# Kernel optimization log

Measured on AMD Instinct MI355X. Metric: run time of the kernel, lower is better.

The kernel has to match this reference:

```python
import jax, jax.numpy as jnp
import numpy as np

B, N, C = 4, 2048, 1024
H = 16
D = C // H
FF = 4096
EPS = 1e-6


def _layernorm(x, g, b):
    mu = jnp.mean(x, axis=-1, keepdims=True)
    var = jnp.mean(jnp.square(x - mu), axis=-1, keepdims=True)
    return (x - mu) * jax.lax.rsqrt(var + EPS) * g + b


def setup_inputs() -> dict:
    key = jax.random.key(0)
    ks = jax.random.split(key, 8)
    s = 0.02
    x = jax.random.normal(ks[0], (B, N, C), dtype=jnp.float32)
    mask = jnp.tril(jnp.ones((N, N), dtype=bool))[None, None]  # causal [1,1,N,N]
    return {
        "x": x,
        "mask": mask,
        "qkv_w": jax.random.normal(ks[1], (3 * C, C), jnp.float32) * s,
        "qkv_b": jnp.zeros((3 * C,), jnp.float32),
        "proj_w": jax.random.normal(ks[2], (C, C), jnp.float32) * s,
        "proj_b": jnp.zeros((C,), jnp.float32),
        "ln1_g": jnp.ones((C,), jnp.float32),
        "ln1_b": jnp.zeros((C,), jnp.float32),
        "ln2_g": jnp.ones((C,), jnp.float32),
        "ln2_b": jnp.zeros((C,), jnp.float32),
        "w1": jax.random.normal(ks[3], (FF, C), jnp.float32) * s,
        "w2": jax.random.normal(ks[4], (C, FF), jnp.float32) * s,
        "w3": jax.random.normal(ks[5], (FF, C), jnp.float32) * s,
    }


def reference(x, mask, qkv_w, qkv_b, proj_w, proj_b, ln1_g, ln1_b, ln2_g, ln2_b, w1, w2, w3):
    # --- attention sub-block (pre-norm) ---
    h = _layernorm(x, ln1_g, ln1_b)
    qkv = h @ qkv_w.T + qkv_b                      # [B,N,3C]
    qkv = qkv.reshape(B, N, 3, H, D).transpose(2, 0, 3, 1, 4)  # [3,B,H,N,D]
    q, k, v = qkv[0], qkv[1], qkv[2]
    scale = D ** -0.5
    attn = jnp.einsum("bhnd,bhmd->bhnm", q, k) * scale
    attn = jnp.where(mask, attn, -jnp.inf)
    attn = jax.nn.softmax(attn, axis=-1)
    o = jnp.einsum("bhnm,bhmd->bhnd", attn, v)
    o = o.transpose(0, 2, 1, 3).reshape(B, N, C)
    o = o @ proj_w.T + proj_b
    x = x + o  # dropout is identity in eval mode
    # --- SwiGLU MLP sub-block (pre-norm) ---
    h = _layernorm(x, ln2_g, ln2_b)
    m = (jax.nn.silu(h @ w1.T) * (h @ w3.T)) @ w2.T
    return x + m
```

## Files before the change

### kernel.cpp

```cpp
#include <hip/hip_runtime.h>
#include <hip/hip_bf16.h>
#include <stdint.h>

#define NB   4
#define NSEQ 2048
#define NC   1024
#define NH   16
#define ND   64
#define NFF  4096
#define NM   (NB*NSEQ)

typedef __attribute__((ext_vector_type(8))) short short8v;
typedef __attribute__((ext_vector_type(4))) short short4v;
typedef __attribute__((ext_vector_type(4))) float f32x4;

#define GPTR(p) ((const __attribute__((address_space(1))) void*)(p))
#define LPTR(p) ((__attribute__((address_space(3))) void*)(p))

__device__ __forceinline__ short f2bf(float f){
  unsigned u = __builtin_bit_cast(unsigned, f);
  u += 0x7fffu + ((u >> 16) & 1u);
  return (short)(u >> 16);
}
__device__ __forceinline__ float bf2f(short h){
  unsigned u = ((unsigned)(unsigned short)h) << 16;
  return __builtin_bit_cast(float, u);
}
__device__ __forceinline__ f32x4 mfma16x32(short8v a, short8v b, f32x4 c){
  return __builtin_amdgcn_mfma_f32_16x16x32_bf16(a, b, c, 0, 0, 0);
}
__device__ __forceinline__ f32x4 mfma16x16(short4v a, short4v b, f32x4 c){
  return __builtin_amdgcn_mfma_f32_16x16x16bf16_1k(a, b, c, 0, 0, 0);
}
__device__ __forceinline__ short4v pack4bf(f32x4 v){
  __hip_bfloat162 a = __float22bfloat162_rn(float2{v[0], v[1]});
  __hip_bfloat162 b = __float22bfloat162_rn(float2{v[2], v[3]});
  short4v r;
  __builtin_memcpy(&r, &a, 4);
  __builtin_memcpy(((char*)&r) + 4, &b, 4);
  return r;
}

__global__ __launch_bounds__(256) void prep_kernel(
    const float* __restrict__ qkv_w, const float* __restrict__ proj_w,
    const float* __restrict__ w1, const float* __restrict__ w3,
    const float* __restrict__ w2,
    short* __restrict__ wqkv, short* __restrict__ wproj,
    short* __restrict__ w1b, short* __restrict__ w3b, short* __restrict__ w2b,
    const float* __restrict__ x, const float* __restrict__ g,
    const float* __restrict__ bta, short* __restrict__ out){
  int blk = blockIdx.x;
  int tid = threadIdx.x;
  if (blk < 16384){
    const float* src; short* dst; int off;
    if      (blk <  3072){ src = qkv_w;  dst = wqkv;  off = blk; }
    else if (blk <  4096){ src = proj_w; dst = wproj; off = blk - 3072; }
    else if (blk <  8192){ src = w1;     dst = w1b;   off = blk - 4096; }
    else if (blk < 12288){ src = w3;     dst = w3b;   off = blk - 8192; }
    else                 { src = w2;     dst = w2b;   off = blk - 12288; }
    int i = (off * 256 + tid) * 4;
    float4 v = *(const float4*)(src + i);
    short4v r = { f2bf(v.x), f2bf(v.y), f2bf(v.z), f2bf(v.w) };
    *(short4v*)(dst + i) = r;
    return;
  }
  int row = blk - 16384;
  int lane = tid & 63, w = tid >> 6;
  const float4* xr = (const float4*)(x + (size_t)row * NC);
  float4 v = xr[tid];
  float s1 = v.x + v.y + v.z + v.w;
  float s2 = v.x*v.x + v.y*v.y + v.z*v.z + v.w*v.w;
  #pragma unroll
  for (int off = 32; off; off >>= 1){
    s1 += __shfl_xor(s1, off);
    s2 += __shfl_xor(s2, off);
  }
  __shared__ float red[8];
  if (lane == 0){ red[w] = s1; red[4 + w] = s2; }
  __syncthreads();
  s1 = red[0] + red[1] + red[2] + red[3];
  s2 = red[4] + red[5] + red[6] + red[7];
  float mean = s1 * (1.0f / NC);
  float var  = s2 * (1.0f / NC) - mean * mean;
  float inv  = rsqrtf(var + 1e-6f);
  float4 gv = ((const float4*)g)[tid];
  float4 bv = ((const float4*)bta)[tid];
  short4v o = { f2bf((v.x - mean) * inv * gv.x + bv.x),
                f2bf((v.y - mean) * inv * gv.y + bv.y),
                f2bf((v.z - mean) * inv * gv.z + bv.z),
                f2bf((v.w - mean) * inv * gv.w + bv.w) };
  *(short4v*)(out + (size_t)row * NC + tid * 4) = o;
}

__global__ __launch_bounds__(256) void ln_kernel(const float* __restrict__ x,
                                                 const float* __restrict__ g,
                                                 const float* __restrict__ bta,
                                                 short* __restrict__ out){
  int row = blockIdx.x;
  int tid = threadIdx.x;
  int lane = tid & 63, w = tid >> 6;
  const float4* xr = (const float4*)(x + (size_t)row * NC);
  float4 v = xr[tid];
  float s1 = v.x + v.y + v.z + v.w;
  float s2 = v.x*v.x + v.y*v.y + v.z*v.z + v.w*v.w;
  #pragma unroll
  for (int off = 32; off; off >>= 1){
    s1 += __shfl_xor(s1, off);
    s2 += __shfl_xor(s2, off);
  }
  __shared__ float red[8];
  if (lane == 0){ red[w] = s1; red[4 + w] = s2; }
  __syncthreads();
  s1 = red[0] + red[1] + red[2] + red[3];
  s2 = red[4] + red[5] + red[6] + red[7];
  float mean = s1 * (1.0f / NC);
  float var  = s2 * (1.0f / NC) - mean * mean;
  float inv  = rsqrtf(var + 1e-6f);
  float4 gv = ((const float4*)g)[tid];
  float4 bv = ((const float4*)bta)[tid];
  short4v o = { f2bf((v.x - mean) * inv * gv.x + bv.x),
                f2bf((v.y - mean) * inv * gv.y + bv.y),
                f2bf((v.z - mean) * inv * gv.z + bv.z),
                f2bf((v.w - mean) * inv * gv.w + bv.w) };
  *(short4v*)(out + (size_t)row * NC + tid * 4) = o;
}

template<bool HAS_BIAS, bool HAS_RES, bool OUT_BF16, bool QKV_V>
__global__ __launch_bounds__(256, 3) void gemm_bt(const short* __restrict__ A,
                                                  const short* __restrict__ Bm,
                                                  const float* __restrict__ bias,
                                                  const float* __restrict__ res,
                                                  void* __restrict__ outp,
                                                  short* __restrict__ vt,
                                                  int Nc, int K){
  __shared__ short Al[128 * 64];
  __shared__ short Bl[128 * 64];
  int tid = threadIdx.x;
  int gx = gridDim.x, nwg = gx * gridDim.y;
  int wg = blockIdx.y * gx + blockIdx.x;
  int swz = (wg & 7) * (nwg >> 3) + (wg >> 3);
  int m0 = (swz / gx) * 128, n0 = (swz % gx) * 128;
  const short* Ag = A + (size_t)m0 * K;
  const short* Bg = Bm + (size_t)n0 * K;
  int lane = tid & 63, wid = tid >> 6;
  int wm = (wid >> 1) * 64, wn = (wid & 1) * 64;
  int qd = lane >> 4, l15 = lane & 15;

  f32x4 acc[4][4] = {};

  for (int k0 = 0; k0 < K; k0 += 64){
    __syncthreads();
    #pragma unroll
    for (int i = 0; i < 4; i++){
      int cg = (wid * 4 + i) * 64 + lane;
      int r  = cg >> 3, c = cg & 7;
      int sc = (c ^ (r & 7)) << 3;
      __builtin_amdgcn_global_load_lds(GPTR(Ag + (size_t)r * K + k0 + sc),
                                       LPTR(&Al[cg * 8]), 16, 0, 0);
      __builtin_amdgcn_global_load_lds(GPTR(Bg + (size_t)r * K + k0 + sc),
                                       LPTR(&Bl[cg * 8]), 16, 0, 0);
    }
    __syncthreads();
    #pragma unroll
    for (int kk = 0; kk < 2; kk++){
      short8v a[4], b[4];
      #pragma unroll
      for (int t = 0; t < 4; t++){
        int r = wm + t * 16 + l15;
        a[t] = *(const short8v*)&Al[r * 64 + (((kk * 4 + qd) ^ (r & 7)) << 3)];
      }
      #pragma unroll
      for (int t = 0; t < 4; t++){
        int r = wn + t * 16 + l15;
        b[t] = *(const short8v*)&Bl[r * 64 + (((kk * 4 + qd) ^ (r & 7)) << 3)];
      }
      #pragma unroll
      for (int i = 0; i < 4; i++)
        #pragma unroll
        for (int j = 0; j < 4; j++)
          acc[i][j] = mfma16x32(a[i], b[j], acc[i][j]);
    }
  }

  #pragma unroll
  for (int ti = 0; ti < 4; ti++){
    #pragma unroll
    for (int tj = 0; tj < 4; tj++){
      int col = n0 + wn + tj * 16 + l15;
      float bv = HAS_BIAS ? bias[col] : 0.0f;
      if (QKV_V && col >= 2048){
        int row0 = m0 + wm + ti * 16 + qd * 4;
        int hh = (col - 2048) >> 6, dd = col & 63;
        int bb = row0 >> 11, nn = row0 & 2047;
        f32x4 v = { acc[ti][tj][0] + bv, acc[ti][tj][1] + bv,
                    acc[ti][tj][2] + bv, acc[ti][tj][3] + bv };
        *(short4v*)(vt + (((size_t)(bb * 16 + hh) * 64 + dd) << 11) + nn) = pack4bf(v);
      } else {
        #pragma unroll
        for (int r = 0; r < 4; r++){
          int row = m0 + wm + ti * 16 + qd * 4 + r;
          float v = acc[ti][tj][r] + bv;
          size_t idx = (size_t)row * Nc + col;
          if (HAS_RES) v += res[idx];
          if (OUT_BF16) ((short*)outp)[idx] = f2bf(v);
          else          ((float*)outp)[idx] = v;
        }
      }
    }
  }
}

__global__ __launch_bounds__(256, 2) void gemm_ff13(const short* __restrict__ A,
                                                    const short* __restrict__ B1m,
                                                    const short* __restrict__ B3m,
                                                    short* __restrict__ outp){
  __shared__ short Al [128 * 64];
  __shared__ short B1l[128 * 64];
  __shared__ short B3l[128 * 64];
  int tid = threadIdx.x;
  int gx = gridDim.x;
  int wg = blockIdx.y * gx + blockIdx.x;
  int xcd = wg & 7, idx = wg >> 3;
  int npx = gx >> 3;
  int n0 = (xcd * npx + idx % npx) * 128;
  int m0 = (idx / npx) * 128;
  const short* Ag  = A   + (size_t)m0 * NC;
  const short* B1g = B1m + (size_t)n0 * NC;
  const short* B3g = B3m + (size_t)n0 * NC;
  int lane = tid & 63, wid = tid >> 6;
  int wm = (wid >> 1) * 64, wn = (wid & 1) * 64;
  int qd = lane >> 4, l15 = lane & 15;

  f32x4 acc1[4][4] = {}, acc3[4][4] = {};

  for (int k0 = 0; k0 < NC; k0 += 64){
    __syncthreads();
    #pragma unroll
    for (int i = 0; i < 4; i++){
      int cg = (wid * 4 + i) * 64 + lane;
      int r  = cg >> 3, c = cg & 7;
      int sc = (c ^ (r & 7)) << 3;
      __builtin_amdgcn_global_load_lds(GPTR(Ag + (size_t)r * NC + k0 + sc),
                                       LPTR(&Al[cg * 8]), 16, 0, 0);
      __builtin_amdgcn_global_load_lds(GPTR(B1g + (size_t)r * NC + k0 + sc),
                                       LPTR(&B1l[cg * 8]), 16, 0, 0);
      __builtin_amdgcn_global_load_lds(GPTR(B3g + (size_t)r * NC + k0 + sc),
                                       LPTR(&B3l[cg * 8]), 16, 0, 0);
    }
    __syncthreads();
    #pragma unroll
    for (int kk = 0; kk < 2; kk++){
      short8v a[4], b1[4], b3[4];
      #pragma unroll
      for (int t = 0; t < 4; t++){
        int r = wm + t * 16 + l15;
        a[t] = *(const short8v*)&Al[r * 64 + (((kk * 4 + qd) ^ (r & 7)) << 3)];
      }
      #pragma unroll
      for (int t = 0; t < 4; t++){
        int r = wn + t * 16 + l15;
        int co = ((kk * 4 + qd) ^ (r & 7)) << 3;
        b1[t] = *(const short8v*)&B1l[r * 64 + co];
        b3[t] = *(const short8v*)&B3l[r * 64 + co];
      }
      #pragma unroll
      for (int i = 0; i < 4; i++)
        #pragma unroll
        for (int j = 0; j < 4; j++){
          acc1[i][j] = mfma16x32(a[i], b1[j], acc1[i][j]);
          acc3[i][j] = mfma16x32(a[i], b3[j], acc3[i][j]);
        }
    }
  }

  #pragma unroll
  for (int ti = 0; ti < 4; ti++){
    #pragma unroll
    for (int tj = 0; tj < 4; tj++){
      int col = n0 + wn + tj * 16 + l15;
      #pragma unroll
      for (int r = 0; r < 4; r++){
        int row = m0 + wm + ti * 16 + qd * 4 + r;
        float v1 = acc1[ti][tj][r];
        float v3 = acc3[ti][tj][r];
        float s = v1 / (1.0f + __expf(-v1)) * v3;
        outp[(size_t)row * NFF + col] = f2bf(s);
      }
    }
  }
}

__global__ __launch_bounds__(256) void attn_kernel(const short* __restrict__ qkvb,
                                                   const short* __restrict__ vt,
                                                   short* __restrict__ outb){
  const float QSCALE = 0.125f * 1.44269504f;
  int bh = blockIdx.x;
  int qb = 15 - blockIdx.y;
  int b = bh >> 4, h = bh & 15;
  int tid = threadIdx.x;
  int lane = tid & 63, wid = tid >> 6;
  int qd = lane >> 4, l15 = lane & 15;
  int qs = qb * 128 + wid * 32;

  const short* qbase = qkvb + (size_t)b * NSEQ * 3072 + h * 64;
  const short* kbase = qbase + 1024;
  const short* vtb   = vt + ((size_t)bh << 17);

  __shared__ short Kl[2][64 * 64];
  __shared__ short Vl[2][64 * 64];

  short8v qf[2][2];
  #pragma unroll
  for (int g = 0; g < 2; g++)
    #pragma unroll
    for (int kc = 0; kc < 2; kc++){
      short8v q = *(const short8v*)(qbase + (size_t)(qs + g * 16 + l15) * 3072
                                    + kc * 32 + qd * 8);
      short8v r;
      #pragma unroll
      for (int j = 0; j < 8; j++) r[j] = f2bf(bf2f(q[j]) * QSCALE);
      qf[g][kc] = r;
    }

  float l_i[2] = { 0.f, 0.f };
  f32x4 o[2][4];
  #pragma unroll
  for (int g = 0; g < 2; g++)
    #pragma unroll
    for (int t = 0; t < 4; t++)
      o[g][t] = (f32x4){0.f, 0.f, 0.f, 0.f};

  int nkt_blk = 2 * qb + 2;
  int itmax   = (qs + 31) >> 6;

  auto STAGE = [&](int bufi, int k0){
    #pragma unroll
    for (int i = 0; i < 2; i++){
      int cg = (wid * 2 + i) * 64 + lane;
      int r  = cg >> 3, c = cg & 7;
      int sc = (c ^ (r & 7)) << 3;
      __builtin_amdgcn_global_load_lds(GPTR(kbase + (size_t)(k0 + r) * 3072 + sc),
                                       LPTR(&Kl[bufi][cg * 8]), 16, 0, 0);
      __builtin_amdgcn_global_load_lds(GPTR(vtb + ((size_t)r << 11) + k0 + sc),
                                       LPTR(&Vl[bufi][cg * 8]), 16, 0, 0);
    }
  };

  STAGE(0, 0);
  __syncthreads();
  int cur = 0;

  for (int it = 0; it < nkt_blk; ++it){
    if (it + 1 < nkt_blk) STAGE(cur ^ 1, (it + 1) * 64);

    if (it <= itmax){
      int k0 = it * 64;
      short8v kf[4][2];
      #pragma unroll
      for (int kt = 0; kt < 4; kt++)
        #pragma unroll
        for (int kc = 0; kc < 2; kc++){
          int r = kt * 16 + l15;
          kf[kt][kc] = *(const short8v*)
              &Kl[cur][r * 64 + (((kc * 4 + qd) ^ (r & 7)) << 3)];
        }
      short4v vf[4][4];
      #pragma unroll
      for (int t = 0; t < 4; t++)
        #pragma unroll
        for (int ks = 0; ks < 4; ks++){
          int r = t * 16 + l15;
          vf[t][ks] = *(const short4v*)
              &Vl[cur][r * 64 + (((ks * 2 + (qd >> 1)) ^ (r & 7)) << 3)
                       + ((qd & 1) << 2)];
        }

      f32x4 s[2][4];
      __builtin_amdgcn_s_setprio(1);
      #pragma unroll
      for (int g = 0; g < 2; g++)
        #pragma unroll
        for (int kt = 0; kt < 4; kt++){
          f32x4 z = (f32x4){0.f, 0.f, 0.f, 0.f};
          z = mfma16x32(kf[kt][0], qf[g][0], z);
          s[g][kt] = mfma16x32(kf[kt][1], qf[g][1], z);
        }
      __builtin_amdgcn_s_setprio(0);

      if (it == itmax){
        #pragma unroll
        for (int g = 0; g < 2; g++){
          int qg = qs + g * 16 + l15;
          #pragma unroll
          for (int kt = 0; kt < 4; kt++)
            #pragma unroll
            for (int r = 0; r < 4; r++){
              int kg = k0 + kt * 16 + qd * 4 + r;
              s[g][kt][r] = (kg <= qg) ? s[g][kt][r] : -1e30f;
            }
        }
      }

      short4v pb[2][4];
      #pragma unroll
      for (int g = 0; g < 2; g++){
        #pragma unroll
        for (int kt = 0; kt < 4; kt++){
          f32x4 p;
          #pragma unroll
          for (int r = 0; r < 4; r++){
            float pv = exp2f(fminf(s[g][kt][r], 24.0f));
            p[r] = pv;
            l_i[g] += pv;
          }
          pb[g][kt] = pack4bf(p);
        }
      }

      __builtin_amdgcn_s_setprio(1);
      #pragma unroll
      for (int g = 0; g < 2; g++)
        #pragma unroll
        for (int t = 0; t < 4; t++)
          #pragma unroll
          for (int ks = 0; ks < 4; ks++)
            o[g][t] = mfma16x16(vf[t][ks], pb[g][ks], o[g][t]);
      __builtin_amdgcn_s_setprio(0);
    }

    __syncthreads();
    cur ^= 1;
  }

  #pragma unroll
  for (int g = 0; g < 2; g++){
    float l = l_i[g];
    l += __shfl_xor(l, 16);
    l += __shfl_xor(l, 32);
    float inv_l = 1.0f / l;
    int q = qs + g * 16 + l15;
    size_t rowbase = ((size_t)(b * NSEQ + q)) * NC + h * 64;
    #pragma unroll
    for (int t = 0; t < 4; t++){
      f32x4 v = { o[g][t][0] * inv_l, o[g][t][1] * inv_l,
                  o[g][t][2] * inv_l, o[g][t][3] * inv_l };
      *(short4v*)(outb + rowbase + t * 16 + qd * 4) = pack4bf(v);
    }
  }
}

extern "C" void kernel_launch(void* const* d_in, const int* in_sizes, int n_in,
                              void* d_out, int out_size, void* d_ws, size_t ws_size,
                              hipStream_t stream){
  const float* x      = (const float*)d_in[0];
  const float* qkv_w  = (const float*)d_in[2];
  const float* qkv_b  = (const float*)d_in[3];
  const float* proj_w = (const float*)d_in[4];
  const float* proj_b = (const float*)d_in[5];
  const float* ln1_g  = (const float*)d_in[6];
  const float* ln1_b  = (const float*)d_in[7];
  const float* ln2_g  = (const float*)d_in[8];
  const float* ln2_b  = (const float*)d_in[9];
  const float* w1     = (const float*)d_in[10];
  const float* w2     = (const float*)d_in[11];
  const float* w3     = (const float*)d_in[12];
  float* out = (float*)d_out;

  short* wqkv  = (short*)d_ws;
  short* wproj = wqkv  + (size_t)3072 * 1024;
  short* w1b   = wproj + (size_t)1024 * 1024;
  short* w3b   = w1b   + (size_t)4096 * 1024;
  short* w2b   = w3b   + (size_t)4096 * 1024;
  short* hb    = w2b   + (size_t)4096 * 1024;
  short* qkvb  = hb    + (size_t)NM * NC;
  short* attnb = qkvb  + (size_t)NM * 3072;
  short* ff3b  = attnb + (size_t)NM * NC;
  float* x1    = (float*)(ff3b + (size_t)NM * NFF);
  short* ff1b  = qkvb;
  short* vtb   = ff3b;

  prep_kernel<<<24576, 256, 0, stream>>>(qkv_w, proj_w, w1, w3, w2,
                                         wqkv, wproj, w1b, w3b, w2b,
                                         x, ln1_g, ln1_b, hb);
  gemm_bt<true, false, true, true><<<dim3(3072 / 128, NM / 128), 256, 0, stream>>>(
      hb, wqkv, qkv_b, nullptr, qkvb, vtb, 3072, 1024);
  attn_kernel<<<dim3(NB * NH, NSEQ / 128), 256, 0, stream>>>(qkvb, vtb, attnb);
  gemm_bt<true, true, false, false><<<dim3(1024 / 128, NM / 128), 256, 0, stream>>>(
      attnb, wproj, proj_b, x, x1, nullptr, 1024, 1024);
  ln_kernel<<<NM, 256, 0, stream>>>(x1, ln2_g, ln2_b, hb);
  gemm_ff13<<<dim3(4096 / 128, NM / 128), 256, 0, stream>>>(hb, w1b, w3b, ff1b);
  gemm_bt<false, true, false, false><<<dim3(1024 / 128, NM / 128), 256, 0, stream>>>(
      ff1b, w2b, nullptr, x1, out, nullptr, 1024, 4096);
}
```

Before: 562.1 us.

## Triple-buffer GEMM K-tiles with async global-to-LDS prefetch and single barrier

Both the generic GEMM and the fused FF1/FF3 GEMM switch from a single-buffered 64-wide K tile with two barriers per step to a three-stage ring of 32-wide K tiles. Loads for tile t+2 are issued while tile t is computed, and vmcnt waits replace the full syncthreads. The XOR swizzle is adapted to the narrower tile, and s_setprio is raised around the MFMA block. The aim is to hide global-memory latency behind compute. The cost is twice as many loop iterations with fewer MFMAs each, plus hand-counted waitcnt values that must match the number of loads in flight.

New measurement: 595.5 us. 5.9% more time.

```diff
diff --git a/kernel.cpp b/kernel.cpp
--- a/kernel.cpp
+++ b/kernel.cpp
@@ -133,8 +133,8 @@
                                                   void* __restrict__ outp,
                                                   short* __restrict__ vt,
                                                   int Nc, int K){
-  __shared__ short Al[128 * 64];
-  __shared__ short Bl[128 * 64];
+  __shared__ short Al[3][128 * 32];
+  __shared__ short Bl[3][128 * 32];
   int tid = threadIdx.x;
   int gx = gridDim.x, nwg = gx * gridDim.y;
   int wg = blockIdx.y * gx + blockIdx.x;
@@ -146,40 +146,53 @@
   int wm = (wid >> 1) * 64, wn = (wid & 1) * 64;
   int qd = lane >> 4, l15 = lane & 15;
 
+  auto STAGE = [&](short* a_, short* b_, int k0){
+    #pragma unroll
+    for (int i = 0; i < 2; i++){
+      int cg = i * 256 + tid;
+      int r = cg >> 2, c = cg & 3;
+      int sc = (c ^ ((r >> 1) & 3)) << 3;
+      __builtin_amdgcn_global_load_lds(GPTR(Ag + (size_t)r * K + k0 + sc),
+                                       LPTR(a_ + cg * 8), 16, 0, 0);
+      __builtin_amdgcn_global_load_lds(GPTR(Bg + (size_t)r * K + k0 + sc),
+                                       LPTR(b_ + cg * 8), 16, 0, 0);
+    }
+  };
+
   f32x4 acc[4][4] = {};
-
-  for (int k0 = 0; k0 < K; k0 += 64){
-    __syncthreads();
-    #pragma unroll
-    for (int i = 0; i < 4; i++){
-      int cg = (wid * 4 + i) * 64 + lane;
-      int r  = cg >> 3, c = cg & 7;
-      int sc = (c ^ (r & 7)) << 3;
-      __builtin_amdgcn_global_load_lds(GPTR(Ag + (size_t)r * K + k0 + sc),
-                                       LPTR(&Al[cg * 8]), 16, 0, 0);
-      __builtin_amdgcn_global_load_lds(GPTR(Bg + (size_t)r * K + k0 + sc),
-                                       LPTR(&Bl[cg * 8]), 16, 0, 0);
-    }
-    __syncthreads();
-    #pragma unroll
-    for (int kk = 0; kk < 2; kk++){
-      short8v a[4], b[4];
-      #pragma unroll
-      for (int t = 0; t < 4; t++){
-        int r = wm + t * 16 + l15;
-        a[t] = *(const short8v*)&Al[r * 64 + (((kk * 4 + qd) ^ (r & 7)) << 3)];
-      }
-      #pragma unroll
-      for (int t = 0; t < 4; t++){
-        int r = wn + t * 16 + l15;
-        b[t] = *(const short8v*)&Bl[r * 64 + (((kk * 4 + qd) ^ (r & 7)) << 3)];
-      }
-      #pragma unroll
-      for (int i = 0; i < 4; i++)
-        #pragma unroll
-        for (int j = 0; j < 4; j++)
-          acc[i][j] = mfma16x32(a[i], b[j], acc[i][j]);
-    }
+  short *A0 = &Al[0][0], *A1 = &Al[1][0], *A2 = &Al[2][0];
+  short *B0 = &Bl[0][0], *B1 = &Bl[1][0], *B2 = &Bl[2][0];
+  int nt = K >> 5;
+  STAGE(A0, B0, 0);
+  STAGE(A1, B1, 32);
+
+  for (int t = 0; t < nt; ++t){
+    if (t + 1 < nt) asm volatile("s_waitcnt vmcnt(4)" ::: "memory");
+    else            asm volatile("s_waitcnt vmcnt(0)" ::: "memory");
+    __builtin_amdgcn_s_barrier();
+    asm volatile("" ::: "memory");
+    __builtin_amdgcn_sched_barrier(0);
+    if (t + 2 < nt) STAGE(A2, B2, (t + 2) * 32);
+    short8v a[4], b[4];
+    #pragma unroll
+    for (int u = 0; u < 4; u++){
+      int r = wm + u * 16 + l15;
+      a[u] = *(const short8v*)&A0[r * 32 + ((qd ^ ((r >> 1) & 3)) << 3)];
+    }
+    #pragma unroll
+    for (int u = 0; u < 4; u++){
+      int r = wn + u * 16 + l15;
+      b[u] = *(const short8v*)&B0[r * 32 + ((qd ^ ((r >> 1) & 3)) << 3)];
+    }
+    __builtin_amdgcn_s_setprio(1);
+    #pragma unroll
+    for (int i = 0; i < 4; i++)
+      #pragma unroll
+      for (int j = 0; j < 4; j++)
+        acc[i][j] = mfma16x32(a[i], b[j], acc[i][j]);
+    __builtin_amdgcn_s_setprio(0);
+    short* tA = A0; A0 = A1; A1 = A2; A2 = tA;
+    short* tB = B0; B0 = B1; B1 = B2; B2 = tB;
   }
 
   #pragma unroll
@@ -214,9 +227,9 @@
                                                     const short* __restrict__ B1m,
                                                     const short* __restrict__ B3m,
                                                     short* __restrict__ outp){
-  __shared__ short Al [128 * 64];
-  __shared__ short B1l[128 * 64];
-  __shared__ short B3l[128 * 64];
+  __shared__ short Al [3][128 * 32];
+  __shared__ short B1l[3][128 * 32];
+  __shared__ short B3l[3][128 * 32];
   int tid = threadIdx.x;
   int gx = gridDim.x;
   int wg = blockIdx.y * gx + blockIdx.x;
@@ -231,46 +244,61 @@
   int wm = (wid >> 1) * 64, wn = (wid & 1) * 64;
   int qd = lane >> 4, l15 = lane & 15;
 
+  auto STAGE = [&](short* a_, short* b1_, short* b3_, int k0){
+    #pragma unroll
+    for (int i = 0; i < 2; i++){
+      int cg = i * 256 + tid;
+      int r = cg >> 2, c = cg & 3;
+      int sc = (c ^ ((r >> 1) & 3)) << 3;
+      __builtin_amdgcn_global_load_lds(GPTR(Ag  + (size_t)r * NC + k0 + sc),
+                                       LPTR(a_  + cg * 8), 16, 0, 0);
+      __builtin_amdgcn_global_load_lds(GPTR(B1g + (size_t)r * NC + k0 + sc),
+                                       LPTR(b1_ + cg * 8), 16, 0, 0);
+      __builtin_amdgcn_global_load_lds(GPTR(B3g + (size_t)r * NC + k0 + sc),
+                                       LPTR(b3_ + cg * 8), 16, 0, 0);
+    }
+  };
+
   f32x4 acc1[4][4] = {}, acc3[4][4] = {};
-
-  for (int k0 = 0; k0 < NC; k0 += 64){
-    __syncthreads();
-    #pragma unroll
-    for (int i = 0; i < 4; i++){
-      int cg = (wid * 4 + i) * 64 + lane;
-      int r  = cg >> 3, c = cg & 7;
-      int sc = (c ^ (r & 7)) << 3;
-      __builtin_amdgcn_global_load_lds(GPTR(Ag + (size_t)r * NC + k0 + sc),
-                                       LPTR(&Al[cg * 8]), 16, 0, 0);
-      __builtin_amdgcn_global_load_lds(GPTR(B1g + (size_t)r * NC + k0 + sc),
-                                       LPTR(&B1l[cg * 8]), 16, 0, 0);
-      __builtin_amdgcn_global_load_lds(GPTR(B3g + (size_t)r * NC + k0 + sc),
-                                       LPTR(&B3l[cg * 8]), 16, 0, 0);
-    }
-    __syncthreads();
-    #pragma unroll
-    for (int kk = 0; kk < 2; kk++){
-      short8v a[4], b1[4], b3[4];
-      #pragma unroll
-      for (int t = 0; t < 4; t++){
-        int r = wm + t * 16 + l15;
-        a[t] = *(const short8v*)&Al[r * 64 + (((kk * 4 + qd) ^ (r & 7)) << 3)];
+  short *A0 = &Al[0][0],  *A1 = &Al[1][0],  *A2 = &Al[2][0];
+  short *C0 = &B1l[0][0], *C1 = &B1l[1][0], *C2 = &B1l[2][0];
+  short *D0 = &B3l[0][0], *D1 = &B3l[1][0], *D2 = &B3l[2][0];
+  const int nt = NC / 32;
+  STAGE(A0, C0, D0, 0);
+  STAGE(A1, C1, D1, 32);
+
+  for (int t = 0; t < nt; ++t){
+    if (t + 1 < nt) asm volatile("s_waitcnt vmcnt(6)" ::: "memory");
+    else            asm volatile("s_waitcnt vmcnt(0)" ::: "memory");
+    __builtin_amdgcn_s_barrier();
+    asm volatile("" ::: "memory");
+    __builtin_amdgcn_sched_barrier(0);
+    if (t + 2 < nt) STAGE(A2, C2, D2, (t + 2) * 32);
+    short8v a[4], c1[4], c3[4];
+    #pragma unroll
+    for (int u = 0; u < 4; u++){
+      int r = wm + u * 16 + l15;
+      a[u] = *(const short8v*)&A0[r * 32 + ((qd ^ ((r >> 1) & 3)) << 3)];
+    }
+    #pragma unroll
+    for (int u = 0; u < 4; u++){
+      int r = wn + u * 16 + l15;
+      int co = (qd ^ ((r >> 1) & 3)) << 3;
+      c1[u] = *(const short8v*)&C0[r * 32 + co];
+      c3[u] = *(const short8v*)&D0[r * 32 + co];
+    }
+    __builtin_amdgcn_s_setprio(1);
+    #pragma unroll
+    for (int i = 0; i < 4; i++)
+      #pragma unroll
+      for (int j = 0; j < 4; j++){
+        acc1[i][j] = mfma16x32(a[i], c1[j], acc1[i][j]);
+        acc3[i][j] = mfma16x32(a[i], c3[j], acc3[i][j]);
       }
-      #pragma unroll
-      for (int t = 0; t < 4; t++){
-        int r = wn + t * 16 + l15;
-        int co = ((kk * 4 + qd) ^ (r & 7)) << 3;
-        b1[t] = *(const short8v*)&B1l[r * 64 + co];
-        b3[t] = *(const short8v*)&B3l[r * 64 + co];
-      }
-      #pragma unroll
-      for (int i = 0; i < 4; i++)
-        #pragma unroll
-        for (int j = 0; j < 4; j++){
-          acc1[i][j] = mfma16x32(a[i], b1[j], acc1[i][j]);
-          acc3[i][j] = mfma16x32(a[i], b3[j], acc3[i][j]);
-        }
-    }
+    __builtin_amdgcn_s_setprio(0);
+    short* t0 = A0; A0 = A1; A1 = A2; A2 = t0;
+    short* t1 = C0; C0 = C1; C1 = C2; C2 = t1;
+    short* t2 = D0; D0 = D1; D1 = D2; D2 = t2;
   }
 
   #pragma unroll
```
